# Kernel optimization log

Hardware: AMD Instinct MI355X
Metric: run time of the kernel (lower is better)

Reference implementation:

```python
import jax, jax.numpy as jnp
import numpy as np
import math

B, NX, NY = 2, 2048, 2048
CX, CY = 1024, 1024
KEY_CH, VAL_CH, HEADS = 1024, 1024, 16


def setup_inputs() -> dict:
    key = jax.random.key(0)
    ks = jax.random.split(key, 10)
    s = lambda fan_in: 1.0 / math.sqrt(fan_in)
    inp = {
        "x": jax.random.normal(ks[0], (B, NX, CX), dtype=jnp.float32),
        "y": jax.random.normal(ks[1], (B, NY, CY), dtype=jnp.float32),
        "Wq": jax.random.uniform(ks[2], (CX, KEY_CH), jnp.float32, -s(CX), s(CX)),
        "bq": jax.random.uniform(ks[3], (KEY_CH,), jnp.float32, -s(CX), s(CX)),
        "Wk": jax.random.uniform(ks[4], (CY, KEY_CH), jnp.float32, -s(CY), s(CY)),
        "bk": jax.random.uniform(ks[5], (KEY_CH,), jnp.float32, -s(CY), s(CY)),
        "Wv": jax.random.uniform(ks[6], (CY, VAL_CH), jnp.float32, -s(CY), s(CY)),
        "bv": jax.random.uniform(ks[7], (VAL_CH,), jnp.float32, -s(CY), s(CY)),
        "Wo": jax.random.uniform(ks[8], (VAL_CH, CX), jnp.float32, -s(VAL_CH), s(VAL_CH)),
        "bo": jax.random.uniform(ks[9], (CX,), jnp.float32, -s(VAL_CH), s(VAL_CH)),
    }
    return inp


def reference(x, y, Wq, bq, Wk, bk, Wv, bv, Wo, bo):
    Bx, Nx, _ = x.shape
    By, Ny, _ = y.shape
    dk = KEY_CH // HEADS
    dv = VAL_CH // HEADS
    # projections
    q = (x @ Wq + bq).reshape(Bx, Nx, HEADS, dk)  # contiguous head slices == reshape
    k = (y @ Wk + bk).reshape(By, Ny, HEADS, dk)
    v = (y @ Wv + bv).reshape(By, Ny, HEADS, dv)
    # NOTE: original scales by 1/sqrt(Ny) (sequence length), not 1/sqrt(dk)
    scores = jnp.einsum("bnhd,bmhd->bhnm", q, k) / jnp.sqrt(jnp.float32(Ny))
    attn = jax.nn.softmax(scores, axis=-1)
    out = jnp.einsum("bhnm,bmhd->bnhd", attn, v).reshape(Bx, Nx, VAL_CH)
    out = jax.nn.relu(out @ Wo + bo)
    # dropout(p=0.2) is identity in eval mode
    return out
```

## Files before the change

### kernel.cpp

```cpp
#include <hip/hip_runtime.h>
#include <hip/hip_bf16.h>

typedef __bf16 bf16;
typedef __attribute__((ext_vector_type(8))) __bf16 bf16x8;
typedef __attribute__((ext_vector_type(4))) __bf16 bf16x4;
typedef __attribute__((ext_vector_type(4))) float f32x4;
typedef __attribute__((ext_vector_type(16))) float f32x16;
typedef __attribute__((ext_vector_type(4))) unsigned int u32x4;

__device__ __forceinline__ void gload_lds16(const void* g, void* l) {
  __builtin_amdgcn_global_load_lds((const __attribute__((address_space(1))) void*)g,
                                   (__attribute__((address_space(3))) void*)l, 16, 0, 0);
}

__device__ __forceinline__ float exp2_fast(float x) {
  float r;
  asm("v_exp_f32 %0, %1" : "=v"(r) : "v"(x));
  return r;
}

__device__ __forceinline__ unsigned cvtpk(float lo, float hi) {
  unsigned r;
  asm("v_cvt_pk_bf16_f32 %0, %1, %2" : "=v"(r) : "v"(lo), "v"(hi));
  return r;
}

__device__ __forceinline__ void plswap(unsigned& a, unsigned& b) {
  asm("v_permlane32_swap_b32 %0, %1" : "+v"(a), "+v"(b));
}

__global__ __launch_bounds__(256) void cvtw_kernel(
    const float* __restrict__ x, const float* __restrict__ y,
    bf16* __restrict__ xb, bf16* __restrict__ yb,
    const float* __restrict__ W0, const float* __restrict__ W1,
    const float* __restrict__ W2, const float* __restrict__ W3,
    bf16* __restrict__ T0, bf16* __restrict__ T1,
    bf16* __restrict__ T2, bf16* __restrict__ T3) {
  __shared__ float t[32][33];
  const int bid = blockIdx.x, tid = threadIdx.x;
  if (bid < 4096) {
    const int z = bid >> 10, rem = bid & 1023;
    const int bx = rem & 31, by = rem >> 5;
    const float* W; bf16* T;
    switch (z) {
      case 0: W = W0; T = T0; break;
      case 1: W = W1; T = T1; break;
      case 2: W = W2; T = T2; break;
      default: W = W3; T = T3; break;
    }
    const int tx = tid & 31, ty = tid >> 5;
    const int bn = bx * 32, bk = by * 32;
#pragma unroll
    for (int i = 0; i < 32; i += 8)
      t[ty + i][tx] = W[(size_t)(bk + ty + i) * 1024 + bn + tx];
    __syncthreads();
#pragma unroll
    for (int i = 0; i < 32; i += 8)
      T[(size_t)(bn + ty + i) * 1024 + bk + tx] = (bf16)t[tx][ty + i];
  } else {
    const int n4 = 1048576;
    int i = (bid - 4096) * 256 + tid;
    const float4* in = (const float4*)x; bf16x4* out = (bf16x4*)xb;
    if (i >= n4) { in = (const float4*)y; out = (bf16x4*)yb; i -= n4; }
    float4 v = in[i];
    bf16x4 o;
    o[0] = (bf16)v.x; o[1] = (bf16)v.y; o[2] = (bf16)v.z; o[3] = (bf16)v.w;
    out[i] = o;
  }
}

__global__ __launch_bounds__(256) void gemm_qkv(
    const bf16* __restrict__ xb, const bf16* __restrict__ yb,
    const bf16* __restrict__ Wqt, const bf16* __restrict__ Wkt, const bf16* __restrict__ Wvt,
    const float* __restrict__ bq, const float* __restrict__ bk, const float* __restrict__ bv,
    bf16* __restrict__ Qb, bf16* __restrict__ Kb, bf16* __restrict__ Vtb) {
  constexpr int K = 1024;
  constexpr float QSCALE = (float)(1.4426950408889634 / 45.254833995939045);
  __shared__ bf16 As[2][128 * 32];
  __shared__ bf16 Bs[2][128 * 32];
  const int z = blockIdx.z;
  const bf16* A  = (z == 0) ? xb : yb;
  const bf16* Bt = (z == 0) ? Wqt : (z == 1) ? Wkt : Wvt;
  const float* bias = (z == 0) ? bq : (z == 1) ? bk : bv;

  const int tid = threadIdx.x;
  const int wave = tid >> 6, lane = tid & 63;
  const int g = lane >> 4, r15 = lane & 15;
  const int m0 = blockIdx.x * 128, n0 = blockIdx.y * 128;
  const int wr = wave >> 1, wc = wave & 1;

  f32x4 acc[4][4] = {};

  const int c0 = tid, c1 = tid + 256;
  const int row0 = c0 >> 2, ch0 = c0 & 3;
  const int row1 = c1 >> 2, ch1 = c1 & 3;

  auto stage = [&](int buf, int k0) {
    gload_lds16(A  + (size_t)(m0 + row0) * K + k0 + ch0 * 8, (char*)As[buf] + c0 * 16);
    gload_lds16(Bt + (size_t)(n0 + row0) * K + k0 + ch0 * 8, (char*)Bs[buf] + c0 * 16);
    gload_lds16(A  + (size_t)(m0 + row1) * K + k0 + ch1 * 8, (char*)As[buf] + c1 * 16);
    gload_lds16(Bt + (size_t)(n0 + row1) * K + k0 + ch1 * 8, (char*)Bs[buf] + c1 * 16);
  };

  stage(0, 0);
  __syncthreads();
  int cur = 0;
  for (int t = 0; t < K / 32; ++t) {
    if (t + 1 < K / 32) stage(cur ^ 1, (t + 1) * 32);
    bf16x8 af[4], bfr[4];
#pragma unroll
    for (int mi = 0; mi < 4; ++mi)
      af[mi] = *(const bf16x8*)((const char*)As[cur] + ((wr * 64 + mi * 16 + r15) * 64 + g * 16));
#pragma unroll
    for (int nj = 0; nj < 4; ++nj)
      bfr[nj] = *(const bf16x8*)((const char*)Bs[cur] + ((wc * 64 + nj * 16 + r15) * 64 + g * 16));
#pragma unroll
    for (int mi = 0; mi < 4; ++mi)
#pragma unroll
      for (int nj = 0; nj < 4; ++nj)
        acc[mi][nj] = __builtin_amdgcn_mfma_f32_16x16x32_bf16(af[mi], bfr[nj], acc[mi][nj], 0, 0, 0);
    __syncthreads();
    cur ^= 1;
  }

  const float scl = (z == 0) ? QSCALE : 1.0f;
#pragma unroll
  for (int mi = 0; mi < 4; ++mi) {
#pragma unroll
    for (int nj = 0; nj < 4; ++nj) {
      int row = m0 + wr * 64 + mi * 16 + g * 4;
      int col = n0 + wc * 64 + nj * 16 + r15;
      float bv_ = bias[col];
      if (z < 2) {
        bf16* C = (z == 0) ? Qb : Kb;
#pragma unroll
        for (int r = 0; r < 4; ++r)
          C[(size_t)(row + r) * 1024 + col] = (bf16)((acc[mi][nj][r] + bv_) * scl);
      } else {
        int b = row >> 11, n = row & 2047;
        bf16x4 pkv;
#pragma unroll
        for (int r = 0; r < 4; ++r)
          pkv[r] = (bf16)(acc[mi][nj][r] + bv_);
        *(bf16x4*)(Vtb + ((size_t)b * 1024 + col) * 2048 + n) = pkv;
      }
    }
  }
}

__global__ __launch_bounds__(256) void gemm_out(
    const bf16* __restrict__ A, const bf16* __restrict__ Bt,
    const float* __restrict__ bias, float* __restrict__ C) {
  constexpr int K = 1024;
  __shared__ bf16 As[2][128 * 32];
  __shared__ bf16 Bs[2][64 * 32];
  const int tid = threadIdx.x;
  const int wave = tid >> 6, lane = tid & 63;
  const int g = lane >> 4, r15 = lane & 15;
  const int m0 = blockIdx.x * 128, n0 = blockIdx.y * 64;
  const int wr = wave >> 1, wc = wave & 1;

  f32x4 acc[4][2] = {};

  const int c0 = tid, c1 = tid + 256;
  const int row0 = c0 >> 2, ch0 = c0 & 3;
  const int row1 = c1 >> 2, ch1 = c1 & 3;

  auto stage = [&](int buf, int k0) {
    gload_lds16(A + (size_t)(m0 + row0) * K + k0 + ch0 * 8, (char*)As[buf] + c0 * 16);
    gload_lds16(A + (size_t)(m0 + row1) * K + k0 + ch1 * 8, (char*)As[buf] + c1 * 16);
    gload_lds16(Bt + (size_t)(n0 + row0) * K + k0 + ch0 * 8, (char*)Bs[buf] + c0 * 16);
  };

  stage(0, 0);
  __syncthreads();
  int cur = 0;
  for (int t = 0; t < K / 32; ++t) {
    if (t + 1 < K / 32) stage(cur ^ 1, (t + 1) * 32);
    bf16x8 af[4], bfr[2];
#pragma unroll
    for (int mi = 0; mi < 4; ++mi)
      af[mi] = *(const bf16x8*)((const char*)As[cur] + ((wr * 64 + mi * 16 + r15) * 64 + g * 16));
#pragma unroll
    for (int nj = 0; nj < 2; ++nj)
      bfr[nj] = *(const bf16x8*)((const char*)Bs[cur] + ((wc * 32 + nj * 16 + r15) * 64 + g * 16));
#pragma unroll
    for (int mi = 0; mi < 4; ++mi)
#pragma unroll
      for (int nj = 0; nj < 2; ++nj)
        acc[mi][nj] = __builtin_amdgcn_mfma_f32_16x16x32_bf16(af[mi], bfr[nj], acc[mi][nj], 0, 0, 0);
    __syncthreads();
    cur ^= 1;
  }

#pragma unroll
  for (int mi = 0; mi < 4; ++mi)
#pragma unroll
    for (int nj = 0; nj < 2; ++nj) {
      int row = m0 + wr * 64 + mi * 16 + g * 4;
      int col = n0 + wc * 32 + nj * 16 + r15;
      float bv_ = bias[col];
#pragma unroll
      for (int r = 0; r < 4; ++r)
        C[(size_t)(row + r) * 1024 + col] = fmaxf(acc[mi][nj][r] + bv_, 0.0f);
    }
}

__global__ __launch_bounds__(128, 2) void attn_kernel(
    const bf16* __restrict__ Q, const bf16* __restrict__ Kin,
    const bf16* __restrict__ Vt, bf16* __restrict__ Oa) {
  __shared__ bf16 Ks[2][64 * 64];
  __shared__ bf16 Vs[2][64 * 64];
  __shared__ float lsh[2][2][32];
  const int tid = threadIdx.x;
  const int w = tid >> 6, lane = tid & 63;
  const int q5 = lane & 31, h = lane >> 5;

  int i = blockIdx.y * 32 + blockIdx.x;
  int xcd = i & 7, slot = i >> 3;
  int bh = xcd * 4 + (slot >> 5), qt = slot & 31;
  int b = bh >> 4, hd = bh & 15;

  const bf16* Qg = Q + ((size_t)b * 2048 + qt * 64) * 1024 + hd * 64;
  const bf16* Kg = Kin + (size_t)b * 2048 * 1024 + hd * 64;
  const bf16* Vg = Vt + ((size_t)b * 1024 + hd * 64) * 2048;

  bf16x8 qf[2][4];
#pragma unroll
  for (int qb = 0; qb < 2; ++qb)
#pragma unroll
    for (int ks = 0; ks < 4; ++ks)
      qf[qb][ks] = *(const bf16x8*)(Qg + (size_t)(qb * 32 + q5) * 1024 + ks * 16 + h * 8);

  f32x16 o[2][2] = {};
  float ls[2] = {};

  auto stage = [&](int buf, int kv0) {
#pragma unroll
    for (int ii = 0; ii < 4; ++ii) {
      int c = tid + ii * 128;
      int row = c >> 3;
      int sl = (c & 7) ^ (row & 7) ^ ((row >> 3) & 1);
      gload_lds16(Kg + (size_t)(kv0 + row) * 1024 + sl * 8, (char*)Ks[buf] + c * 16);
      gload_lds16(Vg + (size_t)row * 2048 + kv0 + sl * 8, (char*)Vs[buf] + c * 16);
    }
  };

  stage(0, 0);
  __syncthreads();
  int cur = 0;

  const int krow = w * 32 + q5;
  const int kswz = (krow & 7) ^ ((krow >> 3) & 1);

  for (int t = 0; t < 32; ++t) {
    if (t < 31) stage(cur ^ 1, (t + 1) * 64);

    f32x16 s[2] = {};
    __builtin_amdgcn_s_setprio(1);
#pragma unroll
    for (int ks = 0; ks < 4; ++ks) {
      bf16x8 kf = *(const bf16x8*)((const char*)Ks[cur] + krow * 128 + (((2 * ks + h) ^ kswz) << 4));
      s[0] = __builtin_amdgcn_mfma_f32_32x32x16_bf16(kf, qf[0][ks], s[0], 0, 0, 0);
      s[1] = __builtin_amdgcn_mfma_f32_32x32x16_bf16(kf, qf[1][ks], s[1], 0, 0, 0);
    }
    __builtin_amdgcn_s_setprio(0);

    unsigned u[2][8];
#pragma unroll
    for (int qb = 0; qb < 2; ++qb) {
      float e[16];
#pragma unroll
      for (int j = 0; j < 16; ++j) e[j] = exp2_fast(s[qb][j]);
      ls[qb] += ((((e[0] + e[1]) + (e[2] + e[3])) + ((e[4] + e[5]) + (e[6] + e[7]))) +
                 (((e[8] + e[9]) + (e[10] + e[11])) + ((e[12] + e[13]) + (e[14] + e[15]))));
#pragma unroll
      for (int p = 0; p < 8; ++p) u[qb][p] = cvtpk(e[2 * p], e[2 * p + 1]);
      plswap(u[qb][0], u[qb][2]); plswap(u[qb][1], u[qb][3]);
      plswap(u[qb][4], u[qb][6]); plswap(u[qb][5], u[qb][7]);
    }

    __builtin_amdgcn_s_setprio(1);
#pragma unroll
    for (int j = 0; j < 2; ++j) {
      const int db = w ^ j;
      const int vrow0 = db * 32 + q5;
      const int vswz = (vrow0 & 7) ^ ((vrow0 >> 3) & 1);
#pragma unroll
      for (int kap = 0; kap < 2; ++kap) {
        bf16x8 vb = *(const bf16x8*)((const char*)Vs[cur] + vrow0 * 128 +
                                     (((4 * w + 2 * kap + h) ^ vswz) << 4));
#pragma unroll
        for (int qb = 0; qb < 2; ++qb) {
          u32x4 uw;
          uw[0] = u[qb][4 * kap + 0]; uw[1] = u[qb][4 * kap + 1];
          uw[2] = u[qb][4 * kap + 2]; uw[3] = u[qb][4 * kap + 3];
          bf16x8 pa = __builtin_bit_cast(bf16x8, uw);
          o[qb][j] = __builtin_amdgcn_mfma_f32_32x32x16_bf16(pa, vb, o[qb][j], 0, 0, 0);
        }
      }
    }
    __builtin_amdgcn_s_setprio(0);

    __syncthreads();
    cur ^= 1;
  }

  ls[0] += __shfl_xor(ls[0], 32);
  ls[1] += __shfl_xor(ls[1], 32);
  if (h == 0) { lsh[w][0][q5] = ls[0]; lsh[w][1][q5] = ls[1]; }

  float* osh = (float*)Ks;
#pragma unroll
  for (int qb = 0; qb < 2; ++qb)
    *(f32x16*)(osh + ((w * 2 + qb) * 64 + lane) * 16) = o[qb][1];
  __syncthreads();

#pragma unroll
  for (int qb = 0; qb < 2; ++qb) {
    float lt = ls[qb] + lsh[1 - w][qb][q5];
    float iv = __builtin_amdgcn_rcpf(lt);
    f32x16 p = *(const f32x16*)(osh + (((1 - w) * 2 + qb) * 64 + lane) * 16);
#pragma unroll
    for (int g4 = 0; g4 < 4; ++g4)
#pragma unroll
      for (int r = 0; r < 4; ++r) {
        int qr = g4 * 8 + 4 * h + r;
        float il = __shfl(iv, qr);
        size_t row = (size_t)b * 2048 + qt * 64 + qb * 32 + qr;
        Oa[row * 1024 + hd * 64 + w * 32 + q5] = (bf16)((o[qb][0][g4 * 4 + r] + p[g4 * 4 + r]) * il);
      }
  }
}

extern "C" void kernel_launch(void* const* d_in, const int* in_sizes, int n_in,
                              void* d_out, int out_size, void* d_ws, size_t ws_size,
                              hipStream_t stream) {
  (void)in_sizes; (void)n_in; (void)out_size; (void)ws_size;
  const float* x  = (const float*)d_in[0];
  const float* y  = (const float*)d_in[1];
  const float* Wq = (const float*)d_in[2];
  const float* bq = (const float*)d_in[3];
  const float* Wk = (const float*)d_in[4];
  const float* bk = (const float*)d_in[5];
  const float* Wv = (const float*)d_in[6];
  const float* bv = (const float*)d_in[7];
  const float* Wo = (const float*)d_in[8];
  const float* bo = (const float*)d_in[9];

  char* ws = (char*)d_ws;
  bf16* xb  = (bf16*)(ws + 0);
  bf16* yb  = (bf16*)(ws + 8388608);
  bf16* Qb  = (bf16*)(ws + 16777216);
  bf16* Kb  = (bf16*)(ws + 25165824);
  bf16* Vtb = (bf16*)(ws + 33554432);
  bf16* Oab = (bf16*)(ws + 41943040);
  bf16* Wqt = (bf16*)(ws + 50331648);
  bf16* Wkt = (bf16*)(ws + 52428800);
  bf16* Wvt = (bf16*)(ws + 54525952);
  bf16* Wot = (bf16*)(ws + 56623104);

  cvtw_kernel<<<12288, 256, 0, stream>>>(x, y, xb, yb, Wq, Wk, Wv, Wo, Wqt, Wkt, Wvt, Wot);
  gemm_qkv<<<dim3(32, 8, 3), 256, 0, stream>>>(xb, yb, Wqt, Wkt, Wvt, bq, bk, bv, Qb, Kb, Vtb);
  attn_kernel<<<dim3(32, 32), dim3(128), 0, stream>>>(Qb, Kb, Vtb, Oab);
  gemm_out<<<dim3(32, 16), 256, 0, stream>>>(Oab, Wot, bo, (float*)d_out);
}
```

Before: 131.6 us.

## Software-pipeline attention loop so PV MFMA of prior tile overlaps softmax exp

New measurement: 129.1 us. Within noise of the previous version (-1.9%).

```diff
diff --git a/kernel.cpp b/kernel.cpp
--- a/kernel.cpp
+++ b/kernel.cpp
@@ -253,8 +253,12 @@
   const int krow = w * 32 + q5;
   const int kswz = (krow & 7) ^ ((krow >> 3) & 1);
 
-  for (int t = 0; t < 32; ++t) {
-    if (t < 31) stage(cur ^ 1, (t + 1) * 64);
+  unsigned uA[2][8], uB[2][8];
+  bf16x8 vA[4], vB[4];
+
+  auto phase = [&](int t, unsigned (&uin)[2][8], unsigned (&uout)[2][8],
+                   bf16x8 (&vin)[4], bf16x8 (&vout)[4], bool doStage, bool doPV) {
+    if (doStage) stage(cur ^ 1, (t + 1) * 64);
 
     f32x16 s[2] = {};
     __builtin_amdgcn_s_setprio(1);
@@ -264,47 +268,69 @@
       s[0] = __builtin_amdgcn_mfma_f32_32x32x16_bf16(kf, qf[0][ks], s[0], 0, 0, 0);
       s[1] = __builtin_amdgcn_mfma_f32_32x32x16_bf16(kf, qf[1][ks], s[1], 0, 0, 0);
     }
-    __builtin_amdgcn_s_setprio(0);
-
-    unsigned u[2][8];
-#pragma unroll
-    for (int qb = 0; qb < 2; ++qb) {
-      float e[16];
-#pragma unroll
-      for (int j = 0; j < 16; ++j) e[j] = exp2_fast(s[qb][j]);
-      ls[qb] += ((((e[0] + e[1]) + (e[2] + e[3])) + ((e[4] + e[5]) + (e[6] + e[7]))) +
-                 (((e[8] + e[9]) + (e[10] + e[11])) + ((e[12] + e[13]) + (e[14] + e[15]))));
-#pragma unroll
-      for (int p = 0; p < 8; ++p) u[qb][p] = cvtpk(e[2 * p], e[2 * p + 1]);
-      plswap(u[qb][0], u[qb][2]); plswap(u[qb][1], u[qb][3]);
-      plswap(u[qb][4], u[qb][6]); plswap(u[qb][5], u[qb][7]);
-    }
-
-    __builtin_amdgcn_s_setprio(1);
+
 #pragma unroll
     for (int j = 0; j < 2; ++j) {
       const int db = w ^ j;
       const int vrow0 = db * 32 + q5;
       const int vswz = (vrow0 & 7) ^ ((vrow0 >> 3) & 1);
 #pragma unroll
-      for (int kap = 0; kap < 2; ++kap) {
-        bf16x8 vb = *(const bf16x8*)((const char*)Vs[cur] + vrow0 * 128 +
-                                     (((4 * w + 2 * kap + h) ^ vswz) << 4));
-#pragma unroll
-        for (int qb = 0; qb < 2; ++qb) {
-          u32x4 uw;
-          uw[0] = u[qb][4 * kap + 0]; uw[1] = u[qb][4 * kap + 1];
-          uw[2] = u[qb][4 * kap + 2]; uw[3] = u[qb][4 * kap + 3];
-          bf16x8 pa = __builtin_bit_cast(bf16x8, uw);
-          o[qb][j] = __builtin_amdgcn_mfma_f32_32x32x16_bf16(pa, vb, o[qb][j], 0, 0, 0);
-        }
-      }
+      for (int kap = 0; kap < 2; ++kap)
+        vout[2 * j + kap] = *(const bf16x8*)((const char*)Vs[cur] + vrow0 * 128 +
+                                             (((4 * w + 2 * kap + h) ^ vswz) << 4));
+    }
+
+    if (doPV) {
+#pragma unroll
+      for (int j = 0; j < 2; ++j)
+#pragma unroll
+        for (int kap = 0; kap < 2; ++kap)
+#pragma unroll
+          for (int qb = 0; qb < 2; ++qb) {
+            u32x4 uw;
+            uw[0] = uin[qb][4 * kap + 0]; uw[1] = uin[qb][4 * kap + 1];
+            uw[2] = uin[qb][4 * kap + 2]; uw[3] = uin[qb][4 * kap + 3];
+            bf16x8 pa = __builtin_bit_cast(bf16x8, uw);
+            o[qb][j] = __builtin_amdgcn_mfma_f32_32x32x16_bf16(pa, vin[2 * j + kap], o[qb][j], 0, 0, 0);
+          }
     }
     __builtin_amdgcn_s_setprio(0);
+
+#pragma unroll
+    for (int qb = 0; qb < 2; ++qb) {
+      float e[16];
+#pragma unroll
+      for (int j = 0; j < 16; ++j) e[j] = exp2_fast(s[qb][j]);
+      ls[qb] += ((((e[0] + e[1]) + (e[2] + e[3])) + ((e[4] + e[5]) + (e[6] + e[7]))) +
+                 (((e[8] + e[9]) + (e[10] + e[11])) + ((e[12] + e[13]) + (e[14] + e[15]))));
+#pragma unroll
+      for (int p = 0; p < 8; ++p) uout[qb][p] = cvtpk(e[2 * p], e[2 * p + 1]);
+      plswap(uout[qb][0], uout[qb][2]); plswap(uout[qb][1], uout[qb][3]);
+      plswap(uout[qb][4], uout[qb][6]); plswap(uout[qb][5], uout[qb][7]);
+    }
 
     __syncthreads();
     cur ^= 1;
-  }
+  };
+
+  phase(0, uB, uA, vB, vA, true, false);
+  for (int t = 1; t < 31; t += 2) {
+    phase(t, uA, uB, vA, vB, true, true);
+    phase(t + 1, uB, uA, vB, vA, true, true);
+  }
+  phase(31, uA, uB, vA, vB, false, true);
+#pragma unroll
+  for (int j = 0; j < 2; ++j)
+#pragma unroll
+    for (int kap = 0; kap < 2; ++kap)
+#pragma unroll
+      for (int qb = 0; qb < 2; ++qb) {
+        u32x4 uw;
+        uw[0] = uB[qb][4 * kap + 0]; uw[1] = uB[qb][4 * kap + 1];
+        uw[2] = uB[qb][4 * kap + 2]; uw[3] = uB[qb][4 * kap + 3];
+        bf16x8 pa = __builtin_bit_cast(bf16x8, uw);
+        o[qb][j] = __builtin_amdgcn_mfma_f32_32x32x16_bf16(pa, vB[2 * j + kap], o[qb][j], 0, 0, 0);
+      }
 
   ls[0] += __shfl_xor(ls[0], 32);
   ls[1] += __shfl_xor(ls[1], 32);
```
